# Optimization experiments

Measured on AMD Instinct MI355X. Metric: run time of the kernel, lower is better.

## Reference

```python
import jax, jax.numpy as jnp
import numpy as np

NEG = -1000000000.0

def _gat(x, adj_pos, W, a_src, a_dst):
    # x: [N,F], W: [H,F], a_src/a_dst: [1,H]
    h = x @ W.T                                          # [N,H]
    e = jax.nn.leaky_relu(h @ a_src.T + (h @ a_dst.T).T, 0.2)  # [N,N] additive attn
    e = jnp.where(adj_pos, e, NEG)
    alpha = jax.nn.softmax(e, axis=-1)
    return alpha @ h                                     # [N,H]

def setup_inputs() -> dict:
    key = jax.random.key(0)
    ks = jax.random.split(key, 24)
    N, F, Cf, C, H = 4096, 64, 10, 64, 128
    s = 0.05
    nrm = lambda k, shp: (jax.random.normal(k, shp, jnp.float32) * s)
    return dict(
        node_features=jax.random.normal(ks[0], (N, F), jnp.float32),
        candidate_features=jax.random.uniform(ks[1], (N, C, Cf), dtype=jnp.float32),
        adjacency=jax.random.randint(ks[2], (N, N), 0, 2).astype(jnp.int32),
        action_mask=jax.random.uniform(ks[3], (N, C), dtype=jnp.float32),
        W1=nrm(ks[4], (H, F)), a1s=nrm(ks[5], (1, H)), a1d=nrm(ks[6], (1, H)),
        W2=nrm(ks[7], (H, H)), a2s=nrm(ks[8], (1, H)), a2d=nrm(ks[9], (1, H)),
        ln_w=jnp.ones((H,), jnp.float32), ln_b=jnp.zeros((H,), jnp.float32),
        Wc1=nrm(ks[10], (H, Cf)), bc1=jnp.zeros((H,), jnp.float32),
        Wc2=nrm(ks[11], (H, H)), bc2=jnp.zeros((H,), jnp.float32),
        Wq=nrm(ks[12], (H, H)), bq=jnp.zeros((H,), jnp.float32),
        Ws1=nrm(ks[13], (H, 2 * H)), bs1=jnp.zeros((H,), jnp.float32),
        Ws2=nrm(ks[14], (1, H)), bs2=jnp.zeros((1,), jnp.float32),
    )

def reference(node_features, candidate_features, adjacency, action_mask,
              W1, a1s, a1d, W2, a2s, a2d, ln_w, ln_b,
              Wc1, bc1, Wc2, bc2, Wq, bq, Ws1, bs1, Ws2, bs2):
    gelu = lambda x: jax.nn.gelu(x, approximate=False)  # torch nn.GELU default (erf)
    adj_pos = adjacency > 0
    # two GAT layers with residual + LayerNorm
    h = jax.nn.relu(_gat(node_features, adj_pos, W1, a1s, a1d))      # [N,H]
    h = jax.nn.relu(_gat(h, adj_pos, W2, a2s, a2d)) + h
    mu = jnp.mean(h, axis=-1, keepdims=True)
    var = jnp.var(h, axis=-1, keepdims=True)
    h = (h - mu) * jax.lax.rsqrt(var + 1e-5) * ln_w + ln_b           # LayerNorm
    # candidate encoder
    cand = gelu(candidate_features @ Wc1.T + bc1)                    # [N,C,H]
    cand = gelu(cand @ Wc2.T + bc2)
    q = (h @ Wq.T + bq)[:, None, :]                                  # [N,1,H]
    fused = jnp.concatenate([q * cand, cand], axis=-1)               # [N,C,2H]
    logits = (gelu(fused @ Ws1.T + bs1) @ Ws2.T + bs2)[..., 0]       # [N,C]
    cf = candidate_features
    bias = (20.0 * cf[..., 0] + 4.0 * cf[..., 4] + 1.5 * cf[..., 5]
            + 1.5 * cf[..., 1] - 1.5 * cf[..., 2]
            + 1.2 * cf[..., 6] + 2.5 * cf[..., 7]
            + 1.6 * cf[..., 8] + 1.2 * cf[..., 9])
    logits = logits + bias
    # rows with no valid action: force action 0 valid
    no_valid = jnp.sum(action_mask, axis=-1) <= 0
    am = action_mask.at[:, 0].set(jnp.where(no_valid, 1.0, action_mask[:, 0]))
    return jnp.where(am > 0, logits, NEG)
```

## Files before the change

### kernel.cpp

```cpp
#include <hip/hip_runtime.h>
#include <hip/hip_bf16.h>
#include <math.h>

#define NN 4096
#define HD 128
#define NCAND 64
#define NCF 10
#define NSEG 16
#define NEGV (-1000000000.0f)

typedef __attribute__((ext_vector_type(8))) short short8_t;
typedef __attribute__((ext_vector_type(4))) float f32x4_t;

__device__ __forceinline__ short f2bf(float f) {
    union { __hip_bfloat16 h; short s; } v;
    v.h = __float2bfloat16(f);
    return v.s;
}
__device__ __forceinline__ float bf2f(short s) {
    union { unsigned u; float f; } v; v.u = ((unsigned)(unsigned short)s) << 16;
    return v.f;
}
__device__ __forceinline__ unsigned pk2(float a, float b) {
    union { __hip_bfloat162 h; unsigned u; } v;
    v.h = __float22bfloat162_rn(make_float2(a, b));
    return v.u;
}

__device__ __forceinline__ float gelu_f(float x) {
    float e = __builtin_amdgcn_exp2f(2.455466f * x);
    float r = __builtin_amdgcn_rcpf(e + 1.0f);
    return x - x * r;
}

__global__ __launch_bounds__(256) void prep_k(
    const int* __restrict__ adj, const float* __restrict__ Wc1,
    const float* __restrict__ Wc2, const float* __restrict__ Ws1,
    unsigned* __restrict__ adjb, short* __restrict__ Wc1b,
    short* __restrict__ Wc2b, short* __restrict__ Wfu)
{
    int tid = threadIdx.x;
    if (blockIdx.x < 2048) {
        long g = (long)blockIdx.x * 256 + tid;
        const int4* p = (const int4*)adj + g * 8;
        unsigned w = 0;
        #pragma unroll
        for (int e = 0; e < 8; ++e) {
            int4 v = p[e];
            w |= (unsigned)(v.x != 0) << (e*4 + 0);
            w |= (unsigned)(v.y != 0) << (e*4 + 1);
            w |= (unsigned)(v.z != 0) << (e*4 + 2);
            w |= (unsigned)(v.w != 0) << (e*4 + 3);
        }
        adjb[g] = w;
    } else {
        int g = (blockIdx.x - 2048) * 256 + tid;
        const int tot = 8 * 256;
        for (int e = g; e < 128*32; e += tot) {
            int t = e >> 5, k = e & 31;
            Wc1b[e] = (k < NCF) ? f2bf(Wc1[t*NCF + k]) : (short)0;
        }
        for (int e = g; e < 128*128; e += tot) {
            int h = e >> 7, pos = e & 127;
            int n = (pos >> 3) | ((pos & 7) << 4);
            Wc2b[e] = f2bf(Wc2[h*128 + n]);
        }
        for (int e = g; e < 128*256; e += tot) {
            int h = e >> 8, j = e & 255;
            int pos = j & 127;
            int n = (pos >> 3) | ((pos & 7) << 4);
            float v = (j < 128) ? Ws1[h*256 + 128 + n] : Ws1[h*256 + n];
            Wfu[e] = f2bf(v);
        }
    }
}

template<int K, int IN, int OUT>
__global__ __launch_bounds__(256) void gatin_k3(
    const float* __restrict__ in, const float* __restrict__ Wf,
    const float* __restrict__ nump, const float* __restrict__ denp,
    float* __restrict__ G1, const float* __restrict__ ln_w,
    const float* __restrict__ ln_b,
    const float* __restrict__ a_s, const float* __restrict__ a_d,
    float* __restrict__ sdv, short* __restrict__ Htb,
    const float* __restrict__ bias, float* __restrict__ outq)
{
    constexpr int AS = K + 4;
    __shared__ float in_s[16*AS];
    __shared__ float H_s[16*132];
    int tid = threadIdx.x;
    int n0 = blockIdx.x * 16;

    if (IN == 0) {
        constexpr int NV = 16*K/4;
        for (int idx = tid; idx < NV; idx += 256) {
            int row = idx / (K/4), c4 = idx - row*(K/4);
            *(float4*)&in_s[row*AS + c4*4] = *(const float4*)&in[(long)(n0+row)*K + c4*4];
        }
    } else {
        int row = tid >> 4, c8 = (tid & 15) * 8;
        float v[8];
        #pragma unroll
        for (int i = 0; i < 8; ++i) v[i] = 0.f;
        float den = 0.f;
        const float* npr = nump + (long)(n0 + row)*NSEG*HD + c8;
        const float* dpr = denp + (long)(n0 + row)*NSEG;
        #pragma unroll
        for (int s = 0; s < NSEG; ++s) {
            const float* np = npr + s*HD;
            float4 a0 = *(const float4*)np;
            float4 a1 = *(const float4*)(np + 4);
            v[0]+=a0.x; v[1]+=a0.y; v[2]+=a0.z; v[3]+=a0.w;
            v[4]+=a1.x; v[5]+=a1.y; v[6]+=a1.z; v[7]+=a1.w;
            den += dpr[s];
        }
        float rd = (den > 0.f) ? __builtin_amdgcn_rcpf(den) : 0.f;
        if (den > 0.f) rd = rd * (2.0f - den * rd);
        #pragma unroll
        for (int i = 0; i < 8; ++i) v[i] = fmaxf(v[i]*rd, 0.f);
        if (IN == 1) {
            float4 o0 = make_float4(v[0],v[1],v[2],v[3]);
            float4 o1 = make_float4(v[4],v[5],v[6],v[7]);
            *(float4*)&G1[(long)(n0+row)*HD + c8]     = o0;
            *(float4*)&G1[(long)(n0+row)*HD + c8 + 4] = o1;
        } else {
            const float* gp = G1 + (long)(n0+row)*HD + c8;
            float4 g0 = *(const float4*)gp;
            float4 g1 = *(const float4*)(gp + 4);
            v[0]+=g0.x; v[1]+=g0.y; v[2]+=g0.z; v[3]+=g0.w;
            v[4]+=g1.x; v[5]+=g1.y; v[6]+=g1.z; v[7]+=g1.w;
            float sm = 0.f, sq = 0.f;
            #pragma unroll
            for (int i = 0; i < 8; ++i) { sm += v[i]; sq += v[i]*v[i]; }
            sm += __shfl_xor(sm,1); sq += __shfl_xor(sq,1);
            sm += __shfl_xor(sm,2); sq += __shfl_xor(sq,2);
            sm += __shfl_xor(sm,4); sq += __shfl_xor(sq,4);
            sm += __shfl_xor(sm,8); sq += __shfl_xor(sq,8);
            float mu  = sm * (1.0f/128.0f);
            float var = sq * (1.0f/128.0f) - mu*mu;
            float nr  = rsqrtf(var + 1e-5f);
            float4 lw0 = *(const float4*)&ln_w[c8];
            float4 lw1 = *(const float4*)&ln_w[c8+4];
            float4 lb0 = *(const float4*)&ln_b[c8];
            float4 lb1 = *(const float4*)&ln_b[c8+4];
            v[0]=(v[0]-mu)*nr*lw0.x+lb0.x; v[1]=(v[1]-mu)*nr*lw0.y+lb0.y;
            v[2]=(v[2]-mu)*nr*lw0.z+lb0.z; v[3]=(v[3]-mu)*nr*lw0.w+lb0.w;
            v[4]=(v[4]-mu)*nr*lw1.x+lb1.x; v[5]=(v[5]-mu)*nr*lw1.y+lb1.y;
            v[6]=(v[6]-mu)*nr*lw1.z+lb1.z; v[7]=(v[7]-mu)*nr*lw1.w+lb1.w;
        }
        #pragma unroll
        for (int i = 0; i < 8; ++i) in_s[row*AS + c8 + i] = v[i];
    }
    __syncthreads();

    int w = tid >> 6, l = tid & 63, l15 = l & 15, qd = l >> 4;
    f32x4_t acc[2];
    acc[0] = (f32x4_t){0.f,0.f,0.f,0.f};
    acc[1] = (f32x4_t){0.f,0.f,0.f,0.f};
    #pragma unroll
    for (int kc = 0; kc < K/32; ++kc) {
        int k0 = kc*32 + qd*8;
        float4 x = *(const float4*)&in_s[l15*AS + k0];
        float4 y = *(const float4*)&in_s[l15*AS + k0 + 4];
        union { short8_t s; unsigned u[4]; } a;
        a.u[0]=pk2(x.x,x.y); a.u[1]=pk2(x.z,x.w);
        a.u[2]=pk2(y.x,y.y); a.u[3]=pk2(y.z,y.w);
        #pragma unroll
        for (int it = 0; it < 2; ++it) {
            int n = (w*2+it)*16 + l15;
            float4 w0 = *(const float4*)&Wf[(long)n*K + k0];
            float4 w1 = *(const float4*)&Wf[(long)n*K + k0 + 4];
            union { short8_t s; unsigned u[4]; } b;
            b.u[0]=pk2(w0.x,w0.y); b.u[1]=pk2(w0.z,w0.w);
            b.u[2]=pk2(w1.x,w1.y); b.u[3]=pk2(w1.z,w1.w);
            acc[it] = __builtin_amdgcn_mfma_f32_16x16x32_bf16(a.s, b.s, acc[it], 0,0,0);
        }
    }

    if (OUT == 1) {
        #pragma unroll
        for (int it = 0; it < 2; ++it) {
            int n = (w*2+it)*16 + l15;
            float bv = bias[n];
            #pragma unroll
            for (int r = 0; r < 4; ++r)
                outq[(long)(n0 + qd*4 + r)*HD + n] = acc[it][r] + bv;
        }
        return;
    }

    #pragma unroll
    for (int it = 0; it < 2; ++it)
        #pragma unroll
        for (int r = 0; r < 4; ++r)
            H_s[(qd*4+r)*132 + (w*2+it)*16 + l15] = acc[it][r];
    __syncthreads();
    {
        int row = tid >> 4, sg = tid & 15;
        int h0 = sg*8;
        float4 as0 = *(const float4*)&a_s[h0];
        float4 as1 = *(const float4*)&a_s[h0+4];
        float4 ad0 = *(const float4*)&a_d[h0];
        float4 ad1 = *(const float4*)&a_d[h0+4];
        float hv[8];
        #pragma unroll
        for (int e = 0; e < 8; ++e) hv[e] = H_s[row*132 + h0 + e];
        float sp = hv[0]*as0.x + hv[1]*as0.y + hv[2]*as0.z + hv[3]*as0.w
                 + hv[4]*as1.x + hv[5]*as1.y + hv[6]*as1.z + hv[7]*as1.w;
        float dp = hv[0]*ad0.x + hv[1]*ad0.y + hv[2]*ad0.z + hv[3]*ad0.w
                 + hv[4]*ad1.x + hv[5]*ad1.y + hv[6]*ad1.z + hv[7]*ad1.w;
        sp += __shfl_xor(sp,1); sp += __shfl_xor(sp,2);
        sp += __shfl_xor(sp,4); sp += __shfl_xor(sp,8);
        dp += __shfl_xor(dp,1); dp += __shfl_xor(dp,2);
        dp += __shfl_xor(dp,4); dp += __shfl_xor(dp,8);
        if (sg == 0) { sdv[n0+row] = sp; sdv[NN + n0 + row] = dp; }
    }
    {
        int h = tid & 127, pr = tid >> 7;
        unsigned u[4];
        #pragma unroll
        for (int c2 = 0; c2 < 4; ++c2)
            u[c2] = pk2(H_s[(pr*8 + 2*c2)*132 + h], H_s[(pr*8 + 2*c2 + 1)*132 + h]);
        *(uint4*)&Htb[(long)h*NN + n0 + pr*8] = make_uint4(u[0],u[1],u[2],u[3]);
    }
}

__global__ __launch_bounds__(256, 4) void agg_k5(
    const unsigned* __restrict__ adjb, const float* __restrict__ sdv,
    const short* __restrict__ Htb, float* __restrict__ num_part,
    float* __restrict__ den_part)
{
    __shared__ __align__(16) short Bs[128*72];
    __shared__ float dj_s[256];
    int tid = threadIdx.x;
    int i0 = blockIdx.x * 32;
    int seg = blockIdx.y;
    int w = tid >> 6, l = tid & 63, l15 = l & 15, qd = l >> 4;
    int mh = w >> 1, nh = w & 1;
    int arow = i0 + mh*16 + l15;
    float si = sdv[arow];
    const float C1 = 1.44269504f;
    const float C2 = 0.28853901f;

    dj_s[tid] = sdv[NN + seg*256 + tid];

    unsigned wbuf[8];
    {
        const uint4* ap = (const uint4*)&adjb[(long)arow*128 + seg*8];
        uint4 q0 = ap[0], q1 = ap[1];
        wbuf[0]=q0.x; wbuf[1]=q0.y; wbuf[2]=q0.z; wbuf[3]=q0.w;
        wbuf[4]=q1.x; wbuf[5]=q1.y; wbuf[6]=q1.z; wbuf[7]=q1.w;
    }

    int sh = tid >> 1, sj = (tid & 1) * 32;
    const short* srcb = Htb + (long)sh*NN + seg*256 + sj;

    f32x4_t acc[4];
    #pragma unroll
    for (int nt = 0; nt < 4; ++nt) acc[nt] = (f32x4_t){0.f,0.f,0.f,0.f};
    float den = 0.f;

    for (int c4 = 0; c4 < 4; ++c4) {
        __syncthreads();
        {
            const uint4* src = (const uint4*)(srcb + c4*64);
            uint4 v0 = src[0], v1 = src[1], v2 = src[2], v3 = src[3];
            uint4* dst = (uint4*)&Bs[sh*72 + sj];
            dst[0]=v0; dst[1]=v1; dst[2]=v2; dst[3]=v3;
        }
        __syncthreads();
        #pragma unroll
        for (int kc = 0; kc < 2; ++kc) {
            int jl = c4*64 + kc*32 + qd*8;
            float4 da = *(const float4*)&dj_s[jl];
            float4 db = *(const float4*)&dj_s[jl+4];
            unsigned byte_ = (wbuf[c4*2+kc] >> (qd*8)) & 0xffu;
            float dv[8] = {da.x,da.y,da.z,da.w,db.x,db.y,db.z,db.w};
            float v[8];
            #pragma unroll
            for (int e = 0; e < 8; ++e) {
                float z = si + dv[e];
                float k = (z > 0.f) ? C1 : C2;
                float wv = __builtin_amdgcn_exp2f(z * k);
                v[e] = ((byte_ >> e) & 1u) ? wv : 0.f;
                den += v[e];
            }
            union { short8_t s; unsigned u[4]; } a;
            a.u[0]=pk2(v[0],v[1]); a.u[1]=pk2(v[2],v[3]);
            a.u[2]=pk2(v[4],v[5]); a.u[3]=pk2(v[6],v[7]);
            int kb = kc*32 + qd*8;
            #pragma unroll
            for (int nt = 0; nt < 4; ++nt) {
                short8_t b = *(const short8_t*)&Bs[(nh*64 + nt*16 + l15)*72 + kb];
                acc[nt] = __builtin_amdgcn_mfma_f32_16x16x32_bf16(a.s, b, acc[nt], 0,0,0);
            }
        }
    }
    den += __shfl_xor(den, 16); den += __shfl_xor(den, 32);
    if (qd == 0 && nh == 0) den_part[(long)arow*NSEG + seg] = den;
    #pragma unroll
    for (int nt = 0; nt < 4; ++nt)
        #pragma unroll
        for (int r = 0; r < 4; ++r)
            num_part[((long)(i0 + mh*16 + qd*4 + r)*NSEG + seg)*HD
                     + nh*64 + nt*16 + l15] = acc[nt][r];
}

__device__ __forceinline__ short8_t mulq2(short8_t c, float4 qa, float4 qb) {
    union { short8_t s; unsigned u[4]; } r;
    r.u[0] = pk2(bf2f(c[0])*qa.x, bf2f(c[1])*qa.y);
    r.u[1] = pk2(bf2f(c[2])*qa.z, bf2f(c[3])*qa.w);
    r.u[2] = pk2(bf2f(c[4])*qb.x, bf2f(c[5])*qb.y);
    r.u[3] = pk2(bf2f(c[6])*qb.z, bf2f(c[7])*qb.w);
    return r.s;
}

__global__ __launch_bounds__(256, 3) void cand_k7(
    const float* __restrict__ cf, const float* __restrict__ am,
    const float* __restrict__ Qb,
    const short* __restrict__ Wc1b, const short* __restrict__ Wc2b,
    const short* __restrict__ Wfu,
    const float* __restrict__ bc1, const float* __restrict__ bc2,
    const float* __restrict__ bs1, const float* __restrict__ Ws2,
    const float* __restrict__ bs2, float* __restrict__ out)
{
    __shared__ __align__(16) short cand_s[128*136];
    __shared__ float bias_s[128];
    __shared__ __align__(16) float q_s[2][128];
    __shared__ float red_s[128*4];
    __shared__ float noval_s[2];
    int tid = threadIdx.x;
    long r0 = (long)blockIdx.x * 128;
    int w = tid >> 6, l = tid & 63, l15 = l & 15, qd = l >> 4;

    {
        float amv = am[r0 + (long)(w >> 1)*64 + l];
        float tot = amv;
        #pragma unroll
        for (int off = 32; off > 0; off >>= 1) tot += __shfl_xor(tot, off);
        if ((w & 1) == 0 && l == 0) noval_s[w >> 1] = (tot <= 0.f) ? 1.f : 0.f;
    }

    {
        int nd = tid >> 7, n = tid & 127;
        float qv = Qb[((r0 >> 6) + nd)*HD + n];
        int pos = ((n & 15) << 3) | (n >> 4);
        q_s[nd][pos] = qv;
    }

    {
        short8_t fa[2];
        #pragma unroll
        for (int im = 0; im < 2; ++im) {
            long row = r0 + (w*2+im)*16 + l15;
            union { short8_t s; unsigned u[4]; } a;
            float bp = 0.f;
            if (qd == 0) {
                float4 x = *(const float4*)&cf[row*10];
                float4 y = *(const float4*)&cf[row*10+4];
                a.u[0]=pk2(x.x,x.y); a.u[1]=pk2(x.z,x.w);
                a.u[2]=pk2(y.x,y.y); a.u[3]=pk2(y.z,y.w);
                bp = 20.0f*x.x + 1.5f*x.y - 1.5f*x.z + 4.0f*y.x
                   + 1.5f*y.y + 1.2f*y.z + 2.5f*y.w;
            } else if (qd == 1) {
                float2 x = *(const float2*)&cf[row*10+8];
                a.u[0]=pk2(x.x,x.y); a.u[1]=0; a.u[2]=0; a.u[3]=0;
                bp = 1.6f*x.x + 1.2f*x.y;
            } else { a.u[0]=a.u[1]=a.u[2]=a.u[3]=0; }
            bp += __shfl_xor(bp, 16);
            if (qd == 0) bias_s[(w*2+im)*16 + l15] = bp;
            fa[im] = a.s;
        }
        f32x4_t acc1[2][8];
        #pragma unroll
        for (int im = 0; im < 2; ++im)
            #pragma unroll
            for (int nt = 0; nt < 8; ++nt) acc1[im][nt] = (f32x4_t){0.f,0.f,0.f,0.f};
        #pragma unroll
        for (int nt = 0; nt < 8; ++nt) {
            short8_t b = *(const short8_t*)&Wc1b[(nt*16 + l15)*32 + qd*8];
            acc1[0][nt] = __builtin_amdgcn_mfma_f32_16x16x32_bf16(fa[0], b, acc1[0][nt], 0,0,0);
            acc1[1][nt] = __builtin_amdgcn_mfma_f32_16x16x32_bf16(fa[1], b, acc1[1][nt], 0,0,0);
        }
        float bv[8];
        #pragma unroll
        for (int nt = 0; nt < 8; ++nt) bv[nt] = bc1[nt*16 + l15];
        #pragma unroll
        for (int im = 0; im < 2; ++im)
            #pragma unroll
            for (int r = 0; r < 4; ++r) {
                unsigned u[4];
                #pragma unroll
                for (int ph = 0; ph < 4; ++ph) {
                    float g0 = gelu_f(acc1[im][2*ph][r]   + bv[2*ph]);
                    float g1 = gelu_f(acc1[im][2*ph+1][r] + bv[2*ph+1]);
                    u[ph] = pk2(g0, g1);
                }
                int m = (w*2+im)*16 + qd*4 + r;
                *(uint4*)&cand_s[m*136 + l15*8] = make_uint4(u[0],u[1],u[2],u[3]);
            }
    }
    __syncthreads();

    f32x4_t acc[8][2];
    #pragma unroll
    for (int mt = 0; mt < 8; ++mt) {
        acc[mt][0] = (f32x4_t){0.f,0.f,0.f,0.f};
        acc[mt][1] = (f32x4_t){0.f,0.f,0.f,0.f};
    }
    #pragma unroll
    for (int kc = 0; kc < 4; ++kc) {
        int kpos = kc*32 + qd*8;
        short8_t a[8];
        #pragma unroll
        for (int mt = 0; mt < 8; ++mt)
            a[mt] = *(const short8_t*)&cand_s[(mt*16 + l15)*136 + kpos];
        short8_t b0 = *(const short8_t*)&Wc2b[((w*2+0)*16 + l15)*128 + kpos];
        short8_t b1 = *(const short8_t*)&Wc2b[((w*2+1)*16 + l15)*128 + kpos];
        #pragma unroll
        for (int mt = 0; mt < 8; ++mt) {
            acc[mt][0] = __builtin_amdgcn_mfma_f32_16x16x32_bf16(a[mt], b0, acc[mt][0], 0,0,0);
            acc[mt][1] = __builtin_amdgcn_mfma_f32_16x16x32_bf16(a[mt], b1, acc[mt][1], 0,0,0);
        }
    }
    __syncthreads();

    {
        float bv0 = bc2[w*32 + l15];
        float bv1 = bc2[w*32 + 16 + l15];
        #pragma unroll
        for (int mt = 0; mt < 8; ++mt)
            #pragma unroll
            for (int r = 0; r < 4; ++r) {
                float g0 = gelu_f(acc[mt][0][r] + bv0);
                float g1 = gelu_f(acc[mt][1][r] + bv1);
                int m = mt*16 + qd*4 + r;
                *(unsigned*)&cand_s[m*136 + l15*8 + w*2] = pk2(g0, g1);
            }
    }
    __syncthreads();

    #pragma unroll
    for (int mt = 0; mt < 8; ++mt) {
        acc[mt][0] = (f32x4_t){0.f,0.f,0.f,0.f};
        acc[mt][1] = (f32x4_t){0.f,0.f,0.f,0.f};
    }
    #pragma unroll
    for (int kc = 0; kc < 4; ++kc) {
        int kpos = kc*32 + qd*8;
        short8_t a[8];
        #pragma unroll
        for (int mt = 0; mt < 8; ++mt)
            a[mt] = *(const short8_t*)&cand_s[(mt*16 + l15)*136 + kpos];
        short8_t b00 = *(const short8_t*)&Wfu[((w*2+0)*16 + l15)*256 + kpos];
        short8_t b10 = *(const short8_t*)&Wfu[((w*2+1)*16 + l15)*256 + kpos];
        short8_t b01 = *(const short8_t*)&Wfu[((w*2+0)*16 + l15)*256 + 128 + kpos];
        short8_t b11 = *(const short8_t*)&Wfu[((w*2+1)*16 + l15)*256 + 128 + kpos];
        float4 qa0 = *(const float4*)&q_s[0][kpos];
        float4 qb0 = *(const float4*)&q_s[0][kpos+4];
        float4 qa1 = *(const float4*)&q_s[1][kpos];
        float4 qb1 = *(const float4*)&q_s[1][kpos+4];
        #pragma unroll
        for (int mt = 0; mt < 8; ++mt) {
            acc[mt][0] = __builtin_amdgcn_mfma_f32_16x16x32_bf16(a[mt], b00, acc[mt][0], 0,0,0);
            acc[mt][1] = __builtin_amdgcn_mfma_f32_16x16x32_bf16(a[mt], b10, acc[mt][1], 0,0,0);
            short8_t aq = (mt < 4) ? mulq2(a[mt], qa0, qb0) : mulq2(a[mt], qa1, qb1);
            acc[mt][0] = __builtin_amdgcn_mfma_f32_16x16x32_bf16(aq, b01, acc[mt][0], 0,0,0);
            acc[mt][1] = __builtin_amdgcn_mfma_f32_16x16x32_bf16(aq, b11, acc[mt][1], 0,0,0);
        }
    }

    {
        float bs1v0 = bs1[w*32 + l15],      bs1v1 = bs1[w*32 + 16 + l15];
        float ws2v0 = Ws2[w*32 + l15],      ws2v1 = Ws2[w*32 + 16 + l15];
        #pragma unroll
        for (int mt = 0; mt < 8; ++mt)
            #pragma unroll
            for (int r = 0; r < 4; ++r) {
                float p = gelu_f(acc[mt][0][r] + bs1v0) * ws2v0
                        + gelu_f(acc[mt][1][r] + bs1v1) * ws2v1;
                p += __shfl_xor(p,1); p += __shfl_xor(p,2);
                p += __shfl_xor(p,4); p += __shfl_xor(p,8);
                if (l15 == 0)
                    red_s[(mt*16 + qd*4 + r)*4 + w] = p;
            }
    }
    __syncthreads();

    if (tid < 128) {
        int m = tid;
        float lg = red_s[m*4] + red_s[m*4+1] + red_s[m*4+2] + red_s[m*4+3]
                 + bs2[0] + bias_s[m];
        float mk = am[r0 + m];
        if ((m & 63) == 0 && noval_s[m >> 6] > 0.f) mk = 1.0f;
        out[r0 + m] = (mk > 0.f) ? lg : NEGV;
    }
}

extern "C" void kernel_launch(void* const* d_in, const int* in_sizes, int n_in,
                              void* d_out, int out_size, void* d_ws, size_t ws_size,
                              hipStream_t stream)
{
    const float* X   = (const float*)d_in[0];
    const float* CF  = (const float*)d_in[1];
    const int*   ADJ = (const int*)d_in[2];
    const float* AM  = (const float*)d_in[3];
    const float* W1  = (const float*)d_in[4];
    const float* A1S = (const float*)d_in[5];
    const float* A1D = (const float*)d_in[6];
    const float* W2  = (const float*)d_in[7];
    const float* A2S = (const float*)d_in[8];
    const float* A2D = (const float*)d_in[9];
    const float* LNW = (const float*)d_in[10];
    const float* LNB = (const float*)d_in[11];
    const float* WC1 = (const float*)d_in[12];
    const float* BC1 = (const float*)d_in[13];
    const float* WC2 = (const float*)d_in[14];
    const float* BC2 = (const float*)d_in[15];
    const float* WQ  = (const float*)d_in[16];
    const float* BQ  = (const float*)d_in[17];
    const float* WS1 = (const float*)d_in[18];
    const float* BS1 = (const float*)d_in[19];
    const float* WS2 = (const float*)d_in[20];
    const float* BS2 = (const float*)d_in[21];
    float* OUT = (float*)d_out;

    float* ws = (float*)d_ws;
    float*    G1   = ws;
    float*    Qb   = ws + 524288;
    float*    sdv  = ws + 1048576;
    float*    denp = ws + 1056768;
    short*    Htb  = (short*)(ws + 1122304);
    unsigned* adjb = (unsigned*)(ws + 1384448);
    short*    Wc1b = (short*)(ws + 1908736);
    short*    Wc2b = (short*)(ws + 1910784);
    short*    Wfu  = (short*)(ws + 1918976);
    float*    nump = ws + 1935360;

    prep_k<<<2056, 256, 0, stream>>>(ADJ, WC1, WC2, WS1, adjb, Wc1b, Wc2b, Wfu);

    gatin_k3<64, 0, 0><<<256, 256, 0, stream>>>(
        X, W1, nullptr, nullptr, nullptr, nullptr, nullptr,
        A1S, A1D, sdv, Htb, nullptr, nullptr);
    agg_k5<<<dim3(128, NSEG), 256, 0, stream>>>(adjb, sdv, Htb, nump, denp);

    gatin_k3<128, 1, 0><<<256, 256, 0, stream>>>(
        nullptr, W2, nump, denp, G1, nullptr, nullptr,
        A2S, A2D, sdv, Htb, nullptr, nullptr);
    agg_k5<<<dim3(128, NSEG), 256, 0, stream>>>(adjb, sdv, Htb, nump, denp);

    gatin_k3<128, 2, 1><<<256, 256, 0, stream>>>(
        nullptr, WQ, nump, denp, G1, LNW, LNB,
        nullptr, nullptr, nullptr, nullptr, BQ, Qb);

    cand_k7<<<2048, 256, 0, stream>>>(CF, AM, Qb, Wc1b, Wc2b, Wfu,
                                      BC1, BC2, BS1, WS2, BS2, OUT);
}
```

Measured before the change: 281.8 us.

## Fold query scaling into fusion weights and double-buffer LDS in aggregation

In the candidate kernel, the elementwise product with q now scales the B-operand weight fragments once per k-chunk instead of every A tile. This relies on the identity (q*cand)·W = cand·(q*W) and cuts the bf16 unpack/multiply/repack work in the MFMA loop. The aggregation kernel gains a double-buffered LDS tile for H, so the next chunk is loaded while the current one is used and one barrier per iteration is dropped, at the cost of twice the LDS. The candidate kernel launch is also split into two half-grid launches through a block offset. Rounding changes slightly because q*W is rounded to bf16 instead of q*cand.

```diff
diff --git a/kernel.cpp b/kernel.cpp
--- a/kernel.cpp
+++ b/kernel.cpp
@@ -225,12 +225,12 @@
     }
 }
 
-__global__ __launch_bounds__(256, 4) void agg_k5(
+__global__ __launch_bounds__(256, 4) void agg_k6(
     const unsigned* __restrict__ adjb, const float* __restrict__ sdv,
     const short* __restrict__ Htb, float* __restrict__ num_part,
     float* __restrict__ den_part)
 {
-    __shared__ __align__(16) short Bs[128*72];
+    __shared__ __align__(16) short Bs[2][128*72];
     __shared__ float dj_s[256];
     int tid = threadIdx.x;
     int i0 = blockIdx.x * 32;
@@ -255,6 +255,13 @@
     int sh = tid >> 1, sj = (tid & 1) * 32;
     const short* srcb = Htb + (long)sh*NN + seg*256 + sj;
 
+    {
+        const uint4* src = (const uint4*)srcb;
+        uint4 v0 = src[0], v1 = src[1], v2 = src[2], v3 = src[3];
+        uint4* dst = (uint4*)&Bs[0][sh*72 + sj];
+        dst[0]=v0; dst[1]=v1; dst[2]=v2; dst[3]=v3;
+    }
+
     f32x4_t acc[4];
     #pragma unroll
     for (int nt = 0; nt < 4; ++nt) acc[nt] = (f32x4_t){0.f,0.f,0.f,0.f};
@@ -262,13 +269,13 @@
 
     for (int c4 = 0; c4 < 4; ++c4) {
         __syncthreads();
-        {
-            const uint4* src = (const uint4*)(srcb + c4*64);
+        if (c4 < 3) {
+            const uint4* src = (const uint4*)(srcb + (c4+1)*64);
             uint4 v0 = src[0], v1 = src[1], v2 = src[2], v3 = src[3];
-            uint4* dst = (uint4*)&Bs[sh*72 + sj];
+            uint4* dst = (uint4*)&Bs[(c4+1)&1][sh*72 + sj];
             dst[0]=v0; dst[1]=v1; dst[2]=v2; dst[3]=v3;
         }
-        __syncthreads();
+        const short* Bcur = Bs[c4&1];
         #pragma unroll
         for (int kc = 0; kc < 2; ++kc) {
             int jl = c4*64 + kc*32 + qd*8;
@@ -291,7 +298,7 @@
             int kb = kc*32 + qd*8;
             #pragma unroll
             for (int nt = 0; nt < 4; ++nt) {
-                short8_t b = *(const short8_t*)&Bs[(nh*64 + nt*16 + l15)*72 + kb];
+                short8_t b = *(const short8_t*)&Bcur[(nh*64 + nt*16 + l15)*72 + kb];
                 acc[nt] = __builtin_amdgcn_mfma_f32_16x16x32_bf16(a.s, b, acc[nt], 0,0,0);
             }
         }
@@ -315,14 +322,14 @@
     return r.s;
 }
 
-__global__ __launch_bounds__(256, 3) void cand_k7(
+__global__ __launch_bounds__(256, 3) void cand_k8(
     const float* __restrict__ cf, const float* __restrict__ am,
     const float* __restrict__ Qb,
     const short* __restrict__ Wc1b, const short* __restrict__ Wc2b,
     const short* __restrict__ Wfu,
     const float* __restrict__ bc1, const float* __restrict__ bc2,
     const float* __restrict__ bs1, const float* __restrict__ Ws2,
-    const float* __restrict__ bs2, float* __restrict__ out)
+    const float* __restrict__ bs2, float* __restrict__ out, int bofs)
 {
     __shared__ __align__(16) short cand_s[128*136];
     __shared__ float bias_s[128];
@@ -330,7 +337,7 @@
     __shared__ float red_s[128*4];
     __shared__ float noval_s[2];
     int tid = threadIdx.x;
-    long r0 = (long)blockIdx.x * 128;
+    long r0 = (long)(blockIdx.x + bofs) * 128;
     int w = tid >> 6, l = tid & 63, l15 = l & 15, qd = l >> 4;
 
     {
@@ -460,13 +467,18 @@
         float4 qb0 = *(const float4*)&q_s[0][kpos+4];
         float4 qa1 = *(const float4*)&q_s[1][kpos];
         float4 qb1 = *(const float4*)&q_s[1][kpos+4];
+        short8_t b01q0 = mulq2(b01, qa0, qb0);
+        short8_t b11q0 = mulq2(b11, qa0, qb0);
+        short8_t b01q1 = mulq2(b01, qa1, qb1);
+        short8_t b11q1 = mulq2(b11, qa1, qb1);
         #pragma unroll
         for (int mt = 0; mt < 8; ++mt) {
+            short8_t bq0 = (mt < 4) ? b01q0 : b01q1;
+            short8_t bq1 = (mt < 4) ? b11q0 : b11q1;
             acc[mt][0] = __builtin_amdgcn_mfma_f32_16x16x32_bf16(a[mt], b00, acc[mt][0], 0,0,0);
             acc[mt][1] = __builtin_amdgcn_mfma_f32_16x16x32_bf16(a[mt], b10, acc[mt][1], 0,0,0);
-            short8_t aq = (mt < 4) ? mulq2(a[mt], qa0, qb0) : mulq2(a[mt], qa1, qb1);
-            acc[mt][0] = __builtin_amdgcn_mfma_f32_16x16x32_bf16(aq, b01, acc[mt][0], 0,0,0);
-            acc[mt][1] = __builtin_amdgcn_mfma_f32_16x16x32_bf16(aq, b11, acc[mt][1], 0,0,0);
+            acc[mt][0] = __builtin_amdgcn_mfma_f32_16x16x32_bf16(a[mt], bq0, acc[mt][0], 0,0,0);
+            acc[mt][1] = __builtin_amdgcn_mfma_f32_16x16x32_bf16(a[mt], bq1, acc[mt][1], 0,0,0);
         }
     }
 
@@ -542,17 +554,19 @@
     gatin_k3<64, 0, 0><<<256, 256, 0, stream>>>(
         X, W1, nullptr, nullptr, nullptr, nullptr, nullptr,
         A1S, A1D, sdv, Htb, nullptr, nullptr);
-    agg_k5<<<dim3(128, NSEG), 256, 0, stream>>>(adjb, sdv, Htb, nump, denp);
+    agg_k6<<<dim3(128, NSEG), 256, 0, stream>>>(adjb, sdv, Htb, nump, denp);
 
     gatin_k3<128, 1, 0><<<256, 256, 0, stream>>>(
         nullptr, W2, nump, denp, G1, nullptr, nullptr,
         A2S, A2D, sdv, Htb, nullptr, nullptr);
-    agg_k5<<<dim3(128, NSEG), 256, 0, stream>>>(adjb, sdv, Htb, nump, denp);
+    agg_k6<<<dim3(128, NSEG), 256, 0, stream>>>(adjb, sdv, Htb, nump, denp);
 
     gatin_k3<128, 2, 1><<<256, 256, 0, stream>>>(
         nullptr, WQ, nump, denp, G1, LNW, LNB,
         nullptr, nullptr, nullptr, nullptr, BQ, Qb);
 
-    cand_k7<<<2048, 256, 0, stream>>>(CF, AM, Qb, Wc1b, Wc2b, Wfu,
-                                      BC1, BC2, BS1, WS2, BS2, OUT);
-}
+    cand_k8<<<1024, 256, 0, stream>>>(CF, AM, Qb, Wc1b, Wc2b, Wfu,
+                                      BC1, BC2, BS1, WS2, BS2, OUT, 0);
+    cand_k8<<<1024, 256, 0, stream>>>(CF, AM, Qb, Wc1b, Wc2b, Wfu,
+                                      BC1, BC2, BS1, WS2, BS2, OUT, 1024);
+}
```

Result: no change. 287.2 us (+1.9%).
